# Performance work log

Hardware: AMD Instinct MI355X
Metric: run time of the kernel (lower is better)

Reference implementation:

```python
import jax, jax.numpy as jnp
import numpy as np

B, T, I, H, O = 64, 2048, 128, 256, 128

def setup_inputs() -> dict:
    key = jax.random.key(0)
    ks = jax.random.split(key, 7)
    return {
        "x": jax.random.normal(ks[0], (B, T, I), dtype=jnp.float32),
        "Wi": jax.random.normal(ks[1], (H, I), dtype=jnp.float32) / np.sqrt(I),
        "bi": jax.random.normal(ks[2], (H,), dtype=jnp.float32) * 0.01,
        "Wh": jax.random.normal(ks[3], (H, H), dtype=jnp.float32) / np.sqrt(H),
        "bh": jax.random.normal(ks[4], (H,), dtype=jnp.float32) * 0.01,
        "Wo": jax.random.normal(ks[5], (O, H), dtype=jnp.float32) / np.sqrt(H),
        "bo": jax.random.normal(ks[6], (O,), dtype=jnp.float32) * 0.01,
    }

def reference(x, Wi, bi, Wh, bh, Wo, bo):
    # x: [B, T, I]; torch Linear weights are [out, in] -> right-multiply by W.T
    b = x.shape[0]
    h0 = jnp.zeros((b, Wh.shape[0]), dtype=x.dtype)
    # precompute input projection for all timesteps (batched GEMM)
    xproj = jnp.einsum('bti,hi->bth', x, Wi) + bi  # [B, T, H]

    def step(h, xp_t):
        h = jnp.tanh(xp_t + h @ Wh.T + bh)
        return h, h

    _, hs = jax.lax.scan(step, h0, jnp.swapaxes(xproj, 0, 1))  # hs: [T, B, H]
    hs = jnp.swapaxes(hs, 0, 1)  # [B, T, H]
    out = jnp.einsum('bth,oh->bto', hs, Wo) + bo  # [B, T, O]
    return out
```

## Files before the change

kernel.cpp:

```cpp
#include <hip/hip_runtime.h>
#include <hip/hip_bf16.h>

#define BB 64
#define TT 2048
#define II 128
#define HH 256
#define OO 128

typedef float f32x4v __attribute__((ext_vector_type(4)));
typedef short bf16x8 __attribute__((ext_vector_type(8)));

#define BM 64
#define BN 64
#define BKT 32

__global__ __launch_bounds__(256) void gemm_f32_bt(
    const float* __restrict__ A, const float* __restrict__ B,
    const float* __restrict__ bias, float* __restrict__ C,
    int M, int N, int K)
{
    __shared__ __align__(16) float As[BKT][BM + 4];
    __shared__ __align__(16) float Bs[BKT][BN + 4];

    const int t  = threadIdx.x;
    const int m0 = blockIdx.x * BM;
    const int n0 = blockIdx.y * BN;
    const int r  = t >> 3;
    const int kq = (t & 7) * 4;
    const int tx = t & 15;
    const int ty = t >> 4;

    float acc[4][4] = {};

    for (int k0 = 0; k0 < K; k0 += BKT) {
        float4 a0 = *(const float4*)&A[(size_t)(m0 + r)      * K + k0 + kq];
        float4 a1 = *(const float4*)&A[(size_t)(m0 + r + 32) * K + k0 + kq];
        float4 b0 = *(const float4*)&B[(size_t)(n0 + r)      * K + k0 + kq];
        float4 b1 = *(const float4*)&B[(size_t)(n0 + r + 32) * K + k0 + kq];

        __syncthreads();
        As[kq + 0][r] = a0.x; As[kq + 1][r] = a0.y; As[kq + 2][r] = a0.z; As[kq + 3][r] = a0.w;
        As[kq + 0][r + 32] = a1.x; As[kq + 1][r + 32] = a1.y; As[kq + 2][r + 32] = a1.z; As[kq + 3][r + 32] = a1.w;
        Bs[kq + 0][r] = b0.x; Bs[kq + 1][r] = b0.y; Bs[kq + 2][r] = b0.z; Bs[kq + 3][r] = b0.w;
        Bs[kq + 0][r + 32] = b1.x; Bs[kq + 1][r + 32] = b1.y; Bs[kq + 2][r + 32] = b1.z; Bs[kq + 3][r + 32] = b1.w;
        __syncthreads();

#pragma unroll
        for (int k = 0; k < BKT; ++k) {
            float4 avv = *(const float4*)&As[k][ty * 4];
            float4 bvv = *(const float4*)&Bs[k][tx * 4];
            const float* av = &avv.x;
            const float* bv = &bvv.x;
#pragma unroll
            for (int i = 0; i < 4; ++i)
#pragma unroll
                for (int j = 0; j < 4; ++j)
                    acc[i][j] = fmaf(av[i], bv[j], acc[i][j]);
        }
    }

#pragma unroll
    for (int i = 0; i < 4; ++i) {
        float4 o;
        o.x = acc[i][0] + bias[n0 + tx * 4 + 0];
        o.y = acc[i][1] + bias[n0 + tx * 4 + 1];
        o.z = acc[i][2] + bias[n0 + tx * 4 + 2];
        o.w = acc[i][3] + bias[n0 + tx * 4 + 3];
        *(float4*)&C[(size_t)(m0 + ty * 4 + i) * N + n0 + tx * 4] = o;
    }
}

typedef unsigned short ushortv4 __attribute__((ext_vector_type(4)));

__device__ __forceinline__ float bf16bits_to_f32(unsigned short u) {
    return __uint_as_float((unsigned)u << 16);
}

__global__ __launch_bounds__(256) void gemm_bf16a_bt(
    const unsigned short* __restrict__ A, const float* __restrict__ B,
    const float* __restrict__ bias, float* __restrict__ C,
    int M, int N, int K)
{
    __shared__ __align__(16) float As[BKT][BM + 4];
    __shared__ __align__(16) float Bs[BKT][BN + 4];

    const int t  = threadIdx.x;
    const int m0 = blockIdx.x * BM;
    const int n0 = blockIdx.y * BN;
    const int r  = t >> 3;
    const int kq = (t & 7) * 4;
    const int kh = kq >> 1;
    const int tx = t & 15;
    const int ty = t >> 4;

    float acc[4][4] = {};

    for (int k0 = 0; k0 < K; k0 += BKT) {
        ushortv4 a0 = *(const ushortv4*)&A[(size_t)(m0 + r)      * K + k0 + kq];
        ushortv4 a1 = *(const ushortv4*)&A[(size_t)(m0 + r + 32) * K + k0 + kq];
        float4  b0 = *(const float4*)&B[(size_t)(n0 + r)      * K + k0 + kq];
        float4  b1 = *(const float4*)&B[(size_t)(n0 + r + 32) * K + k0 + kq];

        __syncthreads();
        As[kh + 0][r]  = bf16bits_to_f32(a0[0]); As[kh + 16][r] = bf16bits_to_f32(a0[1]);
        As[kh + 1][r]  = bf16bits_to_f32(a0[2]); As[kh + 17][r] = bf16bits_to_f32(a0[3]);
        As[kh + 0][r + 32]  = bf16bits_to_f32(a1[0]); As[kh + 16][r + 32] = bf16bits_to_f32(a1[1]);
        As[kh + 1][r + 32]  = bf16bits_to_f32(a1[2]); As[kh + 17][r + 32] = bf16bits_to_f32(a1[3]);
        Bs[kq + 0][r] = b0.x; Bs[kq + 1][r] = b0.y; Bs[kq + 2][r] = b0.z; Bs[kq + 3][r] = b0.w;
        Bs[kq + 0][r + 32] = b1.x; Bs[kq + 1][r + 32] = b1.y; Bs[kq + 2][r + 32] = b1.z; Bs[kq + 3][r + 32] = b1.w;
        __syncthreads();

#pragma unroll
        for (int k = 0; k < BKT; ++k) {
            float4 avv = *(const float4*)&As[k][ty * 4];
            float4 bvv = *(const float4*)&Bs[k][tx * 4];
            const float* av = &avv.x;
            const float* bv = &bvv.x;
#pragma unroll
            for (int i = 0; i < 4; ++i)
#pragma unroll
                for (int j = 0; j < 4; ++j)
                    acc[i][j] = fmaf(av[i], bv[j], acc[i][j]);
        }
    }

#pragma unroll
    for (int i = 0; i < 4; ++i) {
        float4 o;
        o.x = acc[i][0] + bias[n0 + tx * 4 + 0];
        o.y = acc[i][1] + bias[n0 + tx * 4 + 1];
        o.z = acc[i][2] + bias[n0 + tx * 4 + 2];
        o.w = acc[i][3] + bias[n0 + tx * 4 + 3];
        *(float4*)&C[(size_t)(m0 + ty * 4 + i) * N + n0 + tx * 4] = o;
    }
}

#define G 16
#define HPAD 264

__device__ __forceinline__ unsigned short f2bf(float f) {
    union { __hip_bfloat16 h; unsigned short u; } cv;
    cv.h = __float2bfloat16(f);
    return cv.u;
}

__device__ __forceinline__ float tanh_fast(float x) {
    float e = __expf(2.0f * x);
    return 1.0f - 2.0f * __builtin_amdgcn_rcpf(e + 1.0f);
}

__global__ __launch_bounds__(512) __attribute__((amdgpu_waves_per_eu(2, 2)))
void rnn_recurrence_mfma(
    const float* __restrict__ xproj, const float* __restrict__ Wh,
    const float* __restrict__ bh, unsigned short* __restrict__ hs)
{
    __shared__ __align__(16) unsigned short hbl[2][G][HPAD];

    const int blk  = blockIdx.x;
    const int tid  = threadIdx.x;
    const int wave = tid >> 6;
    const int lane = tid & 63;
    const int l15  = lane & 15;
    const int lg   = lane >> 4;
    const int n0   = wave * 32;

#define LOADB(nt, kt, dst) { \
        const float* wp = Wh + (size_t)(n0 + (nt)*16 + l15) * HH + (kt)*32 + lg*4; \
        dst[0] = (short)f2bf(wp[0]);  dst[1] = (short)f2bf(wp[16]); \
        dst[2] = (short)f2bf(wp[1]);  dst[3] = (short)f2bf(wp[17]); \
        dst[4] = (short)f2bf(wp[2]);  dst[5] = (short)f2bf(wp[18]); \
        dst[6] = (short)f2bf(wp[3]);  dst[7] = (short)f2bf(wp[19]); }

    bf16x8 B00, B01, B02, B03, B04, B05, B06, B07;
    bf16x8 B10, B11, B12, B13, B14, B15, B16, B17;
    LOADB(0, 0, B00) LOADB(0, 1, B01) LOADB(0, 2, B02) LOADB(0, 3, B03)
    LOADB(0, 4, B04) LOADB(0, 5, B05) LOADB(0, 6, B06) LOADB(0, 7, B07)
    LOADB(1, 0, B10) LOADB(1, 1, B11) LOADB(1, 2, B12) LOADB(1, 3, B13)
    LOADB(1, 4, B14) LOADB(1, 5, B15) LOADB(1, 6, B16) LOADB(1, 7, B17)

    const float bh0 = bh[n0 + l15];
    const float bh1 = bh[n0 + 16 + l15];

    const int mb = blk * G + lg * 4;
    const float* xq0 = xproj + (size_t)(mb + 0) * TT * HH + n0 + l15;
    const float* xq1 = xproj + (size_t)(mb + 1) * TT * HH + n0 + l15;
    const float* xq2 = xproj + (size_t)(mb + 2) * TT * HH + n0 + l15;
    const float* xq3 = xproj + (size_t)(mb + 3) * TT * HH + n0 + l15;
    unsigned short* hq0 = hs + (size_t)(mb + 0) * TT * HH + n0 + 2 * l15;
    unsigned short* hq1 = hs + (size_t)(mb + 1) * TT * HH + n0 + 2 * l15;
    unsigned short* hq2 = hs + (size_t)(mb + 2) * TT * HH + n0 + 2 * l15;
    unsigned short* hq3 = hs + (size_t)(mb + 3) * TT * HH + n0 + 2 * l15;

    for (int i = tid; i < G * HPAD; i += 512)
        ((unsigned short*)hbl[0])[i] = 0;
    float xv0 = xq0[0],  xv1 = xq1[0],  xv2 = xq2[0],  xv3 = xq3[0];
    float xv4 = xq0[16], xv5 = xq1[16], xv6 = xq2[16], xv7 = xq3[16];
    __syncthreads();

    unsigned int pk0 = 0, pk1 = 0, pk2 = 0, pk3 = 0;

    for (int t = 0; t < TT; ++t) {
        const int p = t & 1;

        const unsigned short* hrow = &hbl[p][l15][lg * 8];
        bf16x8 a0 = *(const bf16x8*)(hrow + 0 * 32);
        bf16x8 a1 = *(const bf16x8*)(hrow + 1 * 32);
        bf16x8 a2 = *(const bf16x8*)(hrow + 2 * 32);
        bf16x8 a3 = *(const bf16x8*)(hrow + 3 * 32);
        bf16x8 a4 = *(const bf16x8*)(hrow + 4 * 32);
        bf16x8 a5 = *(const bf16x8*)(hrow + 5 * 32);
        bf16x8 a6 = *(const bf16x8*)(hrow + 6 * 32);
        bf16x8 a7 = *(const bf16x8*)(hrow + 7 * 32);

        if (t) {
            *(unsigned int*)hq0 = pk0; hq0 += HH;
            *(unsigned int*)hq1 = pk1; hq1 += HH;
            *(unsigned int*)hq2 = pk2; hq2 += HH;
            *(unsigned int*)hq3 = pk3; hq3 += HH;
        }

        f32x4v c00 = {bh0, bh0, bh0, bh0};
        f32x4v c10 = {bh1, bh1, bh1, bh1};
        f32x4v c01 = {xv0, xv1, xv2, xv3};
        f32x4v c11 = {xv4, xv5, xv6, xv7};
        c00 = __builtin_amdgcn_mfma_f32_16x16x32_bf16(a0, B00, c00, 0, 0, 0);
        c10 = __builtin_amdgcn_mfma_f32_16x16x32_bf16(a0, B10, c10, 0, 0, 0);
        c01 = __builtin_amdgcn_mfma_f32_16x16x32_bf16(a4, B04, c01, 0, 0, 0);
        c11 = __builtin_amdgcn_mfma_f32_16x16x32_bf16(a4, B14, c11, 0, 0, 0);
        c00 = __builtin_amdgcn_mfma_f32_16x16x32_bf16(a1, B01, c00, 0, 0, 0);
        c10 = __builtin_amdgcn_mfma_f32_16x16x32_bf16(a1, B11, c10, 0, 0, 0);
        c01 = __builtin_amdgcn_mfma_f32_16x16x32_bf16(a5, B05, c01, 0, 0, 0);
        c11 = __builtin_amdgcn_mfma_f32_16x16x32_bf16(a5, B15, c11, 0, 0, 0);
        c00 = __builtin_amdgcn_mfma_f32_16x16x32_bf16(a2, B02, c00, 0, 0, 0);
        c10 = __builtin_amdgcn_mfma_f32_16x16x32_bf16(a2, B12, c10, 0, 0, 0);
        c01 = __builtin_amdgcn_mfma_f32_16x16x32_bf16(a6, B06, c01, 0, 0, 0);
        c11 = __builtin_amdgcn_mfma_f32_16x16x32_bf16(a6, B16, c11, 0, 0, 0);
        c00 = __builtin_amdgcn_mfma_f32_16x16x32_bf16(a3, B03, c00, 0, 0, 0);
        c10 = __builtin_amdgcn_mfma_f32_16x16x32_bf16(a3, B13, c10, 0, 0, 0);
        c01 = __builtin_amdgcn_mfma_f32_16x16x32_bf16(a7, B07, c01, 0, 0, 0);
        c11 = __builtin_amdgcn_mfma_f32_16x16x32_bf16(a7, B17, c11, 0, 0, 0);

        const int q = (tid >> 5), dummy = q; (void)dummy;
        unsigned int* wr = (unsigned int*)&hbl[p ^ 1][lg * 4][n0 + 2 * l15];
        {
            float h0 = tanh_fast(c00[0] + c01[0]);
            float h1 = tanh_fast(c10[0] + c11[0]);
            asm("v_cvt_pk_bf16_f32 %0, %1, %2" : "=v"(pk0) : "v"(h0), "v"(h1));
            *(unsigned int*)&hbl[p ^ 1][lg * 4 + 0][n0 + 2 * l15] = pk0;
        }
        {
            float h0 = tanh_fast(c00[1] + c01[1]);
            float h1 = tanh_fast(c10[1] + c11[1]);
            asm("v_cvt_pk_bf16_f32 %0, %1, %2" : "=v"(pk1) : "v"(h0), "v"(h1));
            *(unsigned int*)&hbl[p ^ 1][lg * 4 + 1][n0 + 2 * l15] = pk1;
        }
        {
            float h0 = tanh_fast(c00[2] + c01[2]);
            float h1 = tanh_fast(c10[2] + c11[2]);
            asm("v_cvt_pk_bf16_f32 %0, %1, %2" : "=v"(pk2) : "v"(h0), "v"(h1));
            *(unsigned int*)&hbl[p ^ 1][lg * 4 + 2][n0 + 2 * l15] = pk2;
        }
        {
            float h0 = tanh_fast(c00[3] + c01[3]);
            float h1 = tanh_fast(c10[3] + c11[3]);
            asm("v_cvt_pk_bf16_f32 %0, %1, %2" : "=v"(pk3) : "v"(h0), "v"(h1));
            *(unsigned int*)&hbl[p ^ 1][lg * 4 + 3][n0 + 2 * l15] = pk3;
        }
        (void)wr;

        xq0 += HH; xq1 += HH; xq2 += HH; xq3 += HH;
        xv0 = xq0[0];  xv1 = xq1[0];  xv2 = xq2[0];  xv3 = xq3[0];
        xv4 = xq0[16]; xv5 = xq1[16]; xv6 = xq2[16]; xv7 = xq3[16];

        __syncthreads();
    }

    *(unsigned int*)hq0 = pk0;
    *(unsigned int*)hq1 = pk1;
    *(unsigned int*)hq2 = pk2;
    *(unsigned int*)hq3 = pk3;
}

extern "C" void kernel_launch(void* const* d_in, const int* in_sizes, int n_in,
                              void* d_out, int out_size, void* d_ws, size_t ws_size,
                              hipStream_t stream)
{
    const float* x  = (const float*)d_in[0];
    const float* Wi = (const float*)d_in[1];
    const float* bi = (const float*)d_in[2];
    const float* Wh = (const float*)d_in[3];
    const float* bh = (const float*)d_in[4];
    const float* Wo = (const float*)d_in[5];
    const float* bo = (const float*)d_in[6];
    float* out = (float*)d_out;

    const int M = BB * TT;

    float* xproj = (float*)d_ws;
    unsigned short* hs = (unsigned short*)((char*)d_ws + (size_t)M * HH * sizeof(float));

    gemm_f32_bt<<<dim3(M / BM, HH / BN), 256, 0, stream>>>(x, Wi, bi, xproj, M, HH, II);

    rnn_recurrence_mfma<<<dim3(4), 512, 0, stream>>>(xproj, Wh, bh, hs);

    gemm_bf16a_bt<<<dim3(M / BM, OO / BN), 256, 0, stream>>>(
        hs, Wo, bo, out, M, OO, HH);
}
```

Measured before the change: 1.520 ms.

## Fold recurrent bias into input GEMM and interleave xproj layout for recurrence

The input-projection GEMM now adds both bi and bh and writes xproj with columns permuted, so each lane's two hidden units sit next to each other. The recurrence kernel can then read them with one float2 load per row and start the MFMA chain from a single accumulator pair instead of two. This removes the bias accumulators and the extra adds from the serial loop. It also swaps tanh's __expf for a raw v_exp_f32 with a prescaled constant. The trade-off is that the GEMM epilogue now does scalar scattered stores instead of float4 stores, and the K dimension runs as one 8-deep dependent MFMA chain rather than two interleaved 4-deep chains.

```diff
diff --git a/kernel.cpp b/kernel.cpp
--- a/kernel.cpp
+++ b/kernel.cpp
@@ -9,6 +9,23 @@
 
 typedef float f32x4v __attribute__((ext_vector_type(4)));
 typedef short bf16x8 __attribute__((ext_vector_type(8)));
+typedef unsigned short ushortv4 __attribute__((ext_vector_type(4)));
+
+__device__ __forceinline__ float bf16bits_to_f32(unsigned short u) {
+    return __uint_as_float((unsigned)u << 16);
+}
+__device__ __forceinline__ unsigned short f2bf(float f) {
+    union { __hip_bfloat16 h; unsigned short u; } cv;
+    cv.h = __float2bfloat16(f);
+    return cv.u;
+}
+__device__ __forceinline__ float tanh_fast(float x) {
+    float y = x * 2.88539008177793f;
+    float e;
+    asm("v_exp_f32 %0, %1" : "=v"(e) : "v"(y));
+    return 1.0f - 2.0f * __builtin_amdgcn_rcpf(e + 1.0f);
+}
+
 
 #define BM 64
 #define BN 64
@@ -16,8 +33,8 @@
 
 __global__ __launch_bounds__(256) void gemm_f32_bt(
     const float* __restrict__ A, const float* __restrict__ B,
-    const float* __restrict__ bias, float* __restrict__ C,
-    int M, int N, int K)
+    const float* __restrict__ bias, const float* __restrict__ bias2,
+    float* __restrict__ C, int M, int N, int K)
 {
     __shared__ __align__(16) float As[BKT][BM + 4];
     __shared__ __align__(16) float Bs[BKT][BN + 4];
@@ -61,19 +78,14 @@
 
 #pragma unroll
     for (int i = 0; i < 4; ++i) {
-        float4 o;
-        o.x = acc[i][0] + bias[n0 + tx * 4 + 0];
-        o.y = acc[i][1] + bias[n0 + tx * 4 + 1];
-        o.z = acc[i][2] + bias[n0 + tx * 4 + 2];
-        o.w = acc[i][3] + bias[n0 + tx * 4 + 3];
-        *(float4*)&C[(size_t)(m0 + ty * 4 + i) * N + n0 + tx * 4] = o;
-    }
-}
-
-typedef unsigned short ushortv4 __attribute__((ext_vector_type(4)));
-
-__device__ __forceinline__ float bf16bits_to_f32(unsigned short u) {
-    return __uint_as_float((unsigned)u << 16);
+#pragma unroll
+        for (int j = 0; j < 4; ++j) {
+            const int c = n0 + tx * 4 + j;
+            float v = acc[i][j] + bias[c] + bias2[c];
+            const int pos = (c & ~31) + 2 * (c & 15) + ((c & 31) >> 4);
+            C[(size_t)(m0 + ty * 4 + i) * N + pos] = v;
+        }
+    }
 }
 
 __global__ __launch_bounds__(256) void gemm_bf16a_bt(
@@ -138,21 +150,10 @@
 #define G 16
 #define HPAD 264
 
-__device__ __forceinline__ unsigned short f2bf(float f) {
-    union { __hip_bfloat16 h; unsigned short u; } cv;
-    cv.h = __float2bfloat16(f);
-    return cv.u;
-}
-
-__device__ __forceinline__ float tanh_fast(float x) {
-    float e = __expf(2.0f * x);
-    return 1.0f - 2.0f * __builtin_amdgcn_rcpf(e + 1.0f);
-}
-
 __global__ __launch_bounds__(512) __attribute__((amdgpu_waves_per_eu(2, 2)))
 void rnn_recurrence_mfma(
     const float* __restrict__ xproj, const float* __restrict__ Wh,
-    const float* __restrict__ bh, unsigned short* __restrict__ hs)
+    unsigned short* __restrict__ hs)
 {
     __shared__ __align__(16) unsigned short hbl[2][G][HPAD];
 
@@ -178,26 +179,25 @@
     LOADB(1, 0, B10) LOADB(1, 1, B11) LOADB(1, 2, B12) LOADB(1, 3, B13)
     LOADB(1, 4, B14) LOADB(1, 5, B15) LOADB(1, 6, B16) LOADB(1, 7, B17)
 
-    const float bh0 = bh[n0 + l15];
-    const float bh1 = bh[n0 + 16 + l15];
-
     const int mb = blk * G + lg * 4;
-    const float* xq0 = xproj + (size_t)(mb + 0) * TT * HH + n0 + l15;
-    const float* xq1 = xproj + (size_t)(mb + 1) * TT * HH + n0 + l15;
-    const float* xq2 = xproj + (size_t)(mb + 2) * TT * HH + n0 + l15;
-    const float* xq3 = xproj + (size_t)(mb + 3) * TT * HH + n0 + l15;
+    const float* xq0 = xproj + (size_t)(mb + 0) * TT * HH + n0 + 2 * l15;
+    const float* xq1 = xproj + (size_t)(mb + 1) * TT * HH + n0 + 2 * l15;
+    const float* xq2 = xproj + (size_t)(mb + 2) * TT * HH + n0 + 2 * l15;
+    const float* xq3 = xproj + (size_t)(mb + 3) * TT * HH + n0 + 2 * l15;
     unsigned short* hq0 = hs + (size_t)(mb + 0) * TT * HH + n0 + 2 * l15;
     unsigned short* hq1 = hs + (size_t)(mb + 1) * TT * HH + n0 + 2 * l15;
     unsigned short* hq2 = hs + (size_t)(mb + 2) * TT * HH + n0 + 2 * l15;
     unsigned short* hq3 = hs + (size_t)(mb + 3) * TT * HH + n0 + 2 * l15;
 
-    for (int i = tid; i < G * HPAD; i += 512)
-        ((unsigned short*)hbl[0])[i] = 0;
-    float xv0 = xq0[0],  xv1 = xq1[0],  xv2 = xq2[0],  xv3 = xq3[0];
-    float xv4 = xq0[16], xv5 = xq1[16], xv6 = xq2[16], xv7 = xq3[16];
+    for (int i = tid; i < G * HPAD / 2; i += 512)
+        ((unsigned int*)hbl[0])[i] = 0u;
+    float2 xv0 = *(const float2*)xq0;
+    float2 xv1 = *(const float2*)xq1;
+    float2 xv2 = *(const float2*)xq2;
+    float2 xv3 = *(const float2*)xq3;
     __syncthreads();
 
-    unsigned int pk0 = 0, pk1 = 0, pk2 = 0, pk3 = 0;
+    unsigned int sv0 = 0, sv1 = 0, sv2 = 0, sv3 = 0;
 
     for (int t = 0; t < TT; ++t) {
         const int p = t & 1;
@@ -213,72 +213,55 @@
         bf16x8 a7 = *(const bf16x8*)(hrow + 7 * 32);
 
         if (t) {
-            *(unsigned int*)hq0 = pk0; hq0 += HH;
-            *(unsigned int*)hq1 = pk1; hq1 += HH;
-            *(unsigned int*)hq2 = pk2; hq2 += HH;
-            *(unsigned int*)hq3 = pk3; hq3 += HH;
-        }
-
-        f32x4v c00 = {bh0, bh0, bh0, bh0};
-        f32x4v c10 = {bh1, bh1, bh1, bh1};
-        f32x4v c01 = {xv0, xv1, xv2, xv3};
-        f32x4v c11 = {xv4, xv5, xv6, xv7};
-        c00 = __builtin_amdgcn_mfma_f32_16x16x32_bf16(a0, B00, c00, 0, 0, 0);
-        c10 = __builtin_amdgcn_mfma_f32_16x16x32_bf16(a0, B10, c10, 0, 0, 0);
-        c01 = __builtin_amdgcn_mfma_f32_16x16x32_bf16(a4, B04, c01, 0, 0, 0);
-        c11 = __builtin_amdgcn_mfma_f32_16x16x32_bf16(a4, B14, c11, 0, 0, 0);
-        c00 = __builtin_amdgcn_mfma_f32_16x16x32_bf16(a1, B01, c00, 0, 0, 0);
-        c10 = __builtin_amdgcn_mfma_f32_16x16x32_bf16(a1, B11, c10, 0, 0, 0);
-        c01 = __builtin_amdgcn_mfma_f32_16x16x32_bf16(a5, B05, c01, 0, 0, 0);
-        c11 = __builtin_amdgcn_mfma_f32_16x16x32_bf16(a5, B15, c11, 0, 0, 0);
-        c00 = __builtin_amdgcn_mfma_f32_16x16x32_bf16(a2, B02, c00, 0, 0, 0);
-        c10 = __builtin_amdgcn_mfma_f32_16x16x32_bf16(a2, B12, c10, 0, 0, 0);
-        c01 = __builtin_amdgcn_mfma_f32_16x16x32_bf16(a6, B06, c01, 0, 0, 0);
-        c11 = __builtin_amdgcn_mfma_f32_16x16x32_bf16(a6, B16, c11, 0, 0, 0);
-        c00 = __builtin_amdgcn_mfma_f32_16x16x32_bf16(a3, B03, c00, 0, 0, 0);
-        c10 = __builtin_amdgcn_mfma_f32_16x16x32_bf16(a3, B13, c10, 0, 0, 0);
-        c01 = __builtin_amdgcn_mfma_f32_16x16x32_bf16(a7, B07, c01, 0, 0, 0);
-        c11 = __builtin_amdgcn_mfma_f32_16x16x32_bf16(a7, B17, c11, 0, 0, 0);
-
-        const int q = (tid >> 5), dummy = q; (void)dummy;
-        unsigned int* wr = (unsigned int*)&hbl[p ^ 1][lg * 4][n0 + 2 * l15];
-        {
-            float h0 = tanh_fast(c00[0] + c01[0]);
-            float h1 = tanh_fast(c10[0] + c11[0]);
-            asm("v_cvt_pk_bf16_f32 %0, %1, %2" : "=v"(pk0) : "v"(h0), "v"(h1));
-            *(unsigned int*)&hbl[p ^ 1][lg * 4 + 0][n0 + 2 * l15] = pk0;
-        }
-        {
-            float h0 = tanh_fast(c00[1] + c01[1]);
-            float h1 = tanh_fast(c10[1] + c11[1]);
-            asm("v_cvt_pk_bf16_f32 %0, %1, %2" : "=v"(pk1) : "v"(h0), "v"(h1));
-            *(unsigned int*)&hbl[p ^ 1][lg * 4 + 1][n0 + 2 * l15] = pk1;
-        }
-        {
-            float h0 = tanh_fast(c00[2] + c01[2]);
-            float h1 = tanh_fast(c10[2] + c11[2]);
-            asm("v_cvt_pk_bf16_f32 %0, %1, %2" : "=v"(pk2) : "v"(h0), "v"(h1));
-            *(unsigned int*)&hbl[p ^ 1][lg * 4 + 2][n0 + 2 * l15] = pk2;
-        }
-        {
-            float h0 = tanh_fast(c00[3] + c01[3]);
-            float h1 = tanh_fast(c10[3] + c11[3]);
-            asm("v_cvt_pk_bf16_f32 %0, %1, %2" : "=v"(pk3) : "v"(h0), "v"(h1));
-            *(unsigned int*)&hbl[p ^ 1][lg * 4 + 3][n0 + 2 * l15] = pk3;
-        }
-        (void)wr;
+            *(unsigned int*)hq0 = sv0; hq0 += HH;
+            *(unsigned int*)hq1 = sv1; hq1 += HH;
+            *(unsigned int*)hq2 = sv2; hq2 += HH;
+            *(unsigned int*)hq3 = sv3; hq3 += HH;
+        }
+
+        f32x4v c0 = {xv0.x, xv1.x, xv2.x, xv3.x};
+        f32x4v c1 = {xv0.y, xv1.y, xv2.y, xv3.y};
+        c0 = __builtin_amdgcn_mfma_f32_16x16x32_bf16(a0, B00, c0, 0, 0, 0);
+        c1 = __builtin_amdgcn_mfma_f32_16x16x32_bf16(a0, B10, c1, 0, 0, 0);
+        c0 = __builtin_amdgcn_mfma_f32_16x16x32_bf16(a1, B01, c0, 0, 0, 0);
+        c1 = __builtin_amdgcn_mfma_f32_16x16x32_bf16(a1, B11, c1, 0, 0, 0);
+        c0 = __builtin_amdgcn_mfma_f32_16x16x32_bf16(a2, B02, c0, 0, 0, 0);
+        c1 = __builtin_amdgcn_mfma_f32_16x16x32_bf16(a2, B12, c1, 0, 0, 0);
+        c0 = __builtin_amdgcn_mfma_f32_16x16x32_bf16(a3, B03, c0, 0, 0, 0);
+        c1 = __builtin_amdgcn_mfma_f32_16x16x32_bf16(a3, B13, c1, 0, 0, 0);
+        c0 = __builtin_amdgcn_mfma_f32_16x16x32_bf16(a4, B04, c0, 0, 0, 0);
+        c1 = __builtin_amdgcn_mfma_f32_16x16x32_bf16(a4, B14, c1, 0, 0, 0);
+        c0 = __builtin_amdgcn_mfma_f32_16x16x32_bf16(a5, B05, c0, 0, 0, 0);
+        c1 = __builtin_amdgcn_mfma_f32_16x16x32_bf16(a5, B15, c1, 0, 0, 0);
+        c0 = __builtin_amdgcn_mfma_f32_16x16x32_bf16(a6, B06, c0, 0, 0, 0);
+        c1 = __builtin_amdgcn_mfma_f32_16x16x32_bf16(a6, B16, c1, 0, 0, 0);
+        c0 = __builtin_amdgcn_mfma_f32_16x16x32_bf16(a7, B07, c0, 0, 0, 0);
+        c1 = __builtin_amdgcn_mfma_f32_16x16x32_bf16(a7, B17, c1, 0, 0, 0);
+
+#define EPI(r, sv) { \
+        float h0 = tanh_fast(c0[r]); \
+        float h1 = tanh_fast(c1[r]); \
+        asm("v_cvt_pk_bf16_f32 %0, %1, %2" : "=v"(sv) : "v"(h0), "v"(h1)); \
+        *(unsigned int*)&hbl[p ^ 1][lg * 4 + (r)][n0 + 2 * l15] = sv; }
+
+        EPI(0, sv0)
+        EPI(1, sv1)
+        EPI(2, sv2)
+        EPI(3, sv3)
 
         xq0 += HH; xq1 += HH; xq2 += HH; xq3 += HH;
-        xv0 = xq0[0];  xv1 = xq1[0];  xv2 = xq2[0];  xv3 = xq3[0];
-        xv4 = xq0[16]; xv5 = xq1[16]; xv6 = xq2[16]; xv7 = xq3[16];
-
-        __syncthreads();
-    }
-
-    *(unsigned int*)hq0 = pk0;
-    *(unsigned int*)hq1 = pk1;
-    *(unsigned int*)hq2 = pk2;
-    *(unsigned int*)hq3 = pk3;
+        xv0 = *(const float2*)xq0;
+        xv1 = *(const float2*)xq1;
+        xv2 = *(const float2*)xq2;
+        xv3 = *(const float2*)xq3;
+
+        __syncthreads();
+    }
+
+    *(unsigned int*)hq0 = sv0;
+    *(unsigned int*)hq1 = sv1;
+    *(unsigned int*)hq2 = sv2;
+    *(unsigned int*)hq3 = sv3;
 }
 
 extern "C" void kernel_launch(void* const* d_in, const int* in_sizes, int n_in,
@@ -299,9 +282,9 @@
     float* xproj = (float*)d_ws;
     unsigned short* hs = (unsigned short*)((char*)d_ws + (size_t)M * HH * sizeof(float));
 
-    gemm_f32_bt<<<dim3(M / BM, HH / BN), 256, 0, stream>>>(x, Wi, bi, xproj, M, HH, II);
-
-    rnn_recurrence_mfma<<<dim3(4), 512, 0, stream>>>(xproj, Wh, bh, hs);
+    gemm_f32_bt<<<dim3(M / BM, HH / BN), 256, 0, stream>>>(x, Wi, bi, bh, xproj, M, HH, II);
+
+    rnn_recurrence_mfma<<<dim3(4), 512, 0, stream>>>(xproj, Wh, hs);
 
     gemm_bf16a_bt<<<dim3(M / BM, OO / BN), 256, 0, stream>>>(
         hs, Wo, bo, out, M, OO, HH);
```

Measured after the change: 1.410 ms. 1.08x faster.
